# Performance work log

Measured on AMD Instinct MI355X. Metric: run time of the kernel, lower is better.

The kernel has to match this reference:

```python
import jax, jax.numpy as jnp
import numpy as np

EPS_ATTN = 1e-8  # self.eps is undefined in the torch source; standard slot-attention value
LN_EPS = 1e-5


def _ln(x, g=None, b=None, axes=(-1,)):
    m = x.mean(axes, keepdims=True)
    v = ((x - m) ** 2).mean(axes, keepdims=True)
    y = (x - m) * jax.lax.rsqrt(v + LN_EPS)
    return y * g + b if g is not None else y


def setup_inputs() -> dict:
    key = jax.random.key(0)
    ks = jax.random.split(key, 16)
    B, N, S, d, dh = 16, 4096, 8, 64, 128

    def w(k, shape, fan_in):
        return jax.random.normal(k, shape, jnp.float32) / np.float32(np.sqrt(fan_in))

    return {
        "inputs": jax.random.normal(ks[0], (B, N, d + 2), jnp.float32),
        "slots": jax.random.normal(ks[1], (S, d + 4), jnp.float32),
        "Wq": w(ks[2], (d, d), d),
        "Wk": w(ks[3], (d, d), d),
        "Wv": w(ks[4], (d, d), d),
        "Wg": w(ks[5], (d, 2), 2),
        "bg": jnp.zeros((d,), jnp.float32),
        "ln_pos_g": jnp.ones((d,), jnp.float32),
        "ln_pos_b": jnp.zeros((d,), jnp.float32),
        "W1": w(ks[6], (dh, d), d),
        "b1": jnp.zeros((dh,), jnp.float32),
        "W2": w(ks[7], (d, dh), dh),
        "b2": jnp.zeros((d,), jnp.float32),
        "W_ih": w(ks[8], (3 * d, d), d),
        "W_hh": w(ks[9], (3 * d, d), d),
        "b_ih": jnp.zeros((3 * d,), jnp.float32),
        "b_hh": jnp.zeros((3 * d,), jnp.float32),
        "ln_mlp_g": jnp.ones((d,), jnp.float32),
        "ln_mlp_b": jnp.zeros((d,), jnp.float32),
        "W3": w(ks[10], (dh, d), d),
        "b3": jnp.zeros((dh,), jnp.float32),
        "W4": w(ks[11], (d, dh), dh),
        "b4": jnp.zeros((d,), jnp.float32),
        "ln_slot_g": jnp.ones((d,), jnp.float32),
        "ln_slot_b": jnp.zeros((d,), jnp.float32),
        "n_iters": 3,
    }


def reference(inputs, slots, Wq, Wk, Wv, Wg, bg, ln_pos_g, ln_pos_b, W1, b1, W2, b2,
              W_ih, W_hh, b_ih, b_hh, ln_mlp_g, ln_mlp_b, W3, b3, W4, b4,
              ln_slot_g, ln_slot_b, n_iters):
    feats, grids = inputs[..., :-2], inputs[..., -2:]          # (B,N,d), (B,N,2)
    sl, pos, sc = slots[..., :-4], slots[..., -4:-2], slots[..., -2:]
    B, N, _ = feats.shape
    S, d = sl.shape
    scale = d ** (-0.5)

    slots = jnp.broadcast_to(sl, (B, S, d))
    positions = jnp.clip(jnp.broadcast_to(pos, (B, S, 2)), -1.0, 1.0)
    scales = jnp.clip(jnp.broadcast_to(sc, (B, S, 2)), 1e-3, 2.0)

    k = feats @ Wk.T                                           # (B,N,d)
    v = feats @ Wv.T

    def pos_mlp(x):  # LayerNorm -> Linear -> ReLU -> Linear
        h = _ln(x, ln_pos_g, ln_pos_b)
        h = jax.nn.relu(h @ W1.T + b1)
        return h @ W2.T + b2

    for i_iter in range(n_iters + 1):
        rel = (grids[:, :, None] - positions[:, None]) / scales[:, None]  # (B,N,S,2)
        rgp = rel @ Wg.T + bg                                             # (B,N,S,d)
        k_pos = pos_mlp(k[:, :, None] + rgp)                              # (B,N,S,d)
        v_pos = pos_mlp(v[:, :, None] + rgp)

        slots_n = _ln(slots, ln_slot_g, ln_slot_b)
        q = _ln(slots_n, axes=(-2, -1)) @ Wq.T                            # (B,S,d)

        dots = jnp.einsum('bsd,bnsd->bns', q, k_pos) * scale              # (B,N,S)
        attn = jax.nn.softmax(dots, axis=1) + EPS_ATTN
        attn = attn / attn.sum(axis=-1, keepdims=True)

        updates = jnp.einsum('bns,bnsd->bsd', attn, v_pos)                # (B,S,d)
        positions = jnp.einsum('bns,bnp->bsp', attn, grids)               # (B,S,2)
        spread = (grids[:, :, None] - positions[:, None]) ** 2            # (B,N,S,2)
        scales = jnp.clip(jnp.sqrt(jnp.einsum('bns,bnsp->bsp', attn, spread)), 1e-3, 2.0)

        if i_iter < n_iters:
            x = updates.reshape(-1, d)
            h = slots.reshape(-1, d)
            gi = x @ W_ih.T + b_ih
            gh = h @ W_hh.T + b_hh
            i_r, i_z, i_n = jnp.split(gi, 3, axis=-1)
            h_r, h_z, h_n = jnp.split(gh, 3, axis=-1)
            r = jax.nn.sigmoid(i_r + h_r)
            z = jax.nn.sigmoid(i_z + h_z)
            n_g = jnp.tanh(i_n + r * h_n)
            slots = ((1.0 - z) * n_g + z * h).reshape(B, S, d)
            # slot_mlp (no residual in the source)
            hmlp = jax.nn.relu(_ln(slots, ln_mlp_g, ln_mlp_b) @ W3.T + b3)
            slots = hmlp @ W4.T + b4

    return jnp.concatenate([slots, positions, scales], axis=-1)           # (B,S,d+4)
```

## Files before the change

### kernel.cpp

```cpp
#include <hip/hip_runtime.h>
#include <math.h>

#define BB 16
#define NN 4096
#define SS 8
#define DD 64
#define DHH 128
#define CIN 66
#define NITERS 3
#define LN_EPS_F 1e-5f
#define EPS_ATTN_F 1e-8f
#define QSCALE 0.125f

__device__ __forceinline__ float dot4(float4 a, float4 b) {
    return fmaf(a.x, b.x, fmaf(a.y, b.y, fmaf(a.z, b.z, a.w * b.w)));
}

__global__ __launch_bounds__(256) void k_init_slots(
    const float* __restrict__ slots_in, float* __restrict__ slots,
    float* __restrict__ positions, float* __restrict__ scales) {
    int tid = blockIdx.x * 256 + threadIdx.x;
    if (tid < BB * SS * DD) {
        int s = (tid / DD) % SS;
        int c = tid % DD;
        slots[tid] = slots_in[s * 68 + c];
    }
    if (tid < BB * SS * 2) {
        int s = (tid >> 1) & 7;
        int p = tid & 1;
        float po = slots_in[s * 68 + 64 + p];
        positions[tid] = fminf(fmaxf(po, -1.f), 1.f);
        float sc = slots_in[s * 68 + 66 + p];
        scales[tid] = fminf(fmaxf(sc, 1e-3f), 2.f);
    }
}

__global__ __launch_bounds__(256) void k_prep_w(
    const float* __restrict__ W1, const float* __restrict__ lpg,
    const float* __restrict__ lpb, const float* __restrict__ b1,
    const float* __restrict__ Wg,
    float* __restrict__ W1p, float* __restrict__ avec, float* __restrict__ bvec,
    float* __restrict__ s1vec, float* __restrict__ b1p, float* __restrict__ wgc) {
    __shared__ float w1s[128 * 68];
    int tid = threadIdx.x;
    for (int q = 0; q < 8; q++) {
        int flat = q * 1024 + tid * 4;
        int o = flat >> 6, c = flat & 63;
        *(float4*)(w1s + o * 68 + c) = *(const float4*)(W1 + flat);
    }
    __syncthreads();
    if (tid < 128) {
        int o = tid;
        float a = 0.f, bv = 0.f, s1 = 0.f, b1a = b1[o];
        for (int c = 0; c < 64; c++) {
            float w0 = w1s[o * 68 + c];
            float w = w0 * lpg[c];
            W1p[o * 64 + c] = w;
            a = fmaf(w, Wg[2 * c], a);
            bv = fmaf(w, Wg[2 * c + 1], bv);
            s1 += w;
            b1a = fmaf(w0, lpb[c], b1a);
        }
        avec[o] = a; bvec[o] = bv; s1vec[o] = s1; b1p[o] = b1a;
    }
    if (tid == 128) {
        float mwA = 0.f, mwB = 0.f, AA = 0.f, BBv = 0.f, AB = 0.f;
        for (int c = 0; c < 64; c++) {
            float wa = Wg[2 * c], wb = Wg[2 * c + 1];
            mwA += wa; mwB += wb;
            AA = fmaf(wa, wa, AA); BBv = fmaf(wb, wb, BBv); AB = fmaf(wa, wb, AB);
        }
        wgc[0] = mwA * (1.f / 64.f);
        wgc[1] = mwB * (1.f / 64.f);
        wgc[2] = AA * (1.f / 64.f);
        wgc[3] = BBv * (1.f / 64.f);
        wgc[4] = AB * (2.f / 64.f);
    }
}

__global__ __launch_bounds__(256) void k_prep_w2(
    const float* __restrict__ W1p, const float* __restrict__ Wk,
    const float* __restrict__ Wv, const float* __restrict__ bg,
    float* __restrict__ Wall, float* __restrict__ cu) {
    int flat = blockIdx.x * 256 + threadIdx.x;
    int mat = flat >> 13, rem = flat & 8191;
    int o = rem >> 6, c = rem & 63;
    const float* Wm = mat ? Wv : Wk;
    float acc = 0.f;
    for (int d = 0; d < 64; d++)
        acc = fmaf(W1p[o * 64 + d], Wm[d * 64 + c], acc);
    Wall[flat] = acc;
    if (flat < 128) {
        float a = 0.f;
        for (int d = 0; d < 64; d++) a = fmaf(W1p[flat * 64 + d], bg[d], a);
        cu[flat] = a;
    }
}

__global__ __launch_bounds__(256) void k_prep_main(
    const float* __restrict__ inp, const float* __restrict__ Wall,
    const float* __restrict__ cu, const float* __restrict__ Wk,
    const float* __restrict__ Wv, const float* __restrict__ bg,
    const float* __restrict__ Wg,
    float* __restrict__ uk, float* __restrict__ uv,
    float* __restrict__ kaux, float* __restrict__ vaux, float* __restrict__ gbuf) {
    __shared__ float A[64 * 68];
    __shared__ float Bw[128 * 68];
    __shared__ float wg2[132];
    __shared__ float bgs[64];
    __shared__ float cus[128];
    int tid = threadIdx.x;
    int chunk = blockIdx.y;
    int rowBase = blockIdx.x * 64;
    {
        int r = tid >> 2, cq = (tid & 3) * 16;
        const float* src = inp + (size_t)(rowBase + r) * CIN + cq;
        float* dst = A + r * 68 + cq;
        #pragma unroll
        for (int q = 0; q < 8; q++) {
            float2 tv = *(const float2*)(src + 2 * q);
            dst[2 * q] = tv.x; dst[2 * q + 1] = tv.y;
        }
    }
    if (chunk < 2) {
        const float* Wsrc = Wall + (size_t)chunk * 8192;
        int o = tid >> 1, c0 = (tid & 1) * 32;
        #pragma unroll
        for (int q = 0; q < 8; q++)
            *(float4*)(Bw + o * 68 + c0 + 4 * q) = *(const float4*)(Wsrc + o * 64 + c0 + 4 * q);
        if (tid < 128) cus[tid] = cu[tid];
    } else {
        int o = tid >> 1, c0 = (tid & 1) * 32;
        const float* Wsrc = (o < 64) ? (Wk + o * 64) : (Wv + (o - 64) * 64);
        #pragma unroll
        for (int q = 0; q < 8; q++)
            *(float4*)(Bw + o * 68 + c0 + 4 * q) = *(const float4*)(Wsrc + c0 + 4 * q);
        if (tid < 64) {
            wg2[tid] = Wg[2 * tid]; wg2[66 + tid] = Wg[2 * tid + 1];
            bgs[tid] = bg[tid];
        }
    }
    __syncthreads();
    int r4 = tid >> 4, j = tid & 15;
    float acc[4][8];
    #pragma unroll
    for (int rr = 0; rr < 4; rr++)
        #pragma unroll
        for (int q = 0; q < 8; q++) acc[rr][q] = 0.f;
    for (int c4 = 0; c4 < 64; c4 += 4) {
        float4 av[4];
        #pragma unroll
        for (int rr = 0; rr < 4; rr++)
            av[rr] = *(const float4*)(A + (r4 + 16 * rr) * 68 + c4);
        #pragma unroll
        for (int q = 0; q < 8; q++) {
            float4 w = *(const float4*)(Bw + (16 * q + j) * 68 + c4);
            #pragma unroll
            for (int rr = 0; rr < 4; rr++) acc[rr][q] += dot4(av[rr], w);
        }
    }
    if (chunk < 2) {
        float cub[8];
        #pragma unroll
        for (int q = 0; q < 8; q++) cub[q] = cus[16 * q + j];
        __syncthreads();
        #pragma unroll
        for (int rr = 0; rr < 4; rr++)
            #pragma unroll
            for (int q = 0; q < 8; q++)
                Bw[(r4 + 16 * rr) * 132 + 16 * q + j] = acc[rr][q] + cub[q];
        __syncthreads();
        float* dst = (chunk == 0) ? uk : uv;
        int r = tid >> 2, c0 = (tid & 3) * 32;
        #pragma unroll
        for (int q = 0; q < 8; q++)
            *(float4*)(dst + (size_t)(rowBase + r) * 128 + c0 + 4 * q) =
                *(const float4*)(Bw + r * 132 + c0 + 4 * q);
    } else {
        float wa[4], wb[4], bgk[4];
        #pragma unroll
        for (int q = 0; q < 4; q++) {
            int ch = 16 * q + j;
            wa[q] = wg2[ch]; wb[q] = wg2[66 + ch]; bgk[q] = bgs[ch];
        }
        #pragma unroll
        for (int rr = 0; rr < 4; rr++) {
            float mk = 0.f, kk = 0.f, kA = 0.f, kB = 0.f;
            float mv = 0.f, vv = 0.f, vA = 0.f, vB = 0.f;
            #pragma unroll
            for (int q = 0; q < 4; q++) {
                float x = acc[rr][q] + bgk[q];
                mk += x; kk = fmaf(x, x, kk); kA = fmaf(x, wa[q], kA); kB = fmaf(x, wb[q], kB);
                float y = acc[rr][q + 4] + bgk[q];
                mv += y; vv = fmaf(y, y, vv); vA = fmaf(y, wa[q], vA); vB = fmaf(y, wb[q], vB);
            }
            #pragma unroll
            for (int off = 1; off <= 8; off <<= 1) {
                mk += __shfl_xor(mk, off, 64); kk += __shfl_xor(kk, off, 64);
                kA += __shfl_xor(kA, off, 64); kB += __shfl_xor(kB, off, 64);
                mv += __shfl_xor(mv, off, 64); vv += __shfl_xor(vv, off, 64);
                vA += __shfl_xor(vA, off, 64); vB += __shfl_xor(vB, off, 64);
            }
            if (j == 0) {
                int row = rowBase + r4 + 16 * rr;
                float g0 = inp[(size_t)row * CIN + 64];
                float g1 = inp[(size_t)row * CIN + 65];
                float4 m1 = {mk * (1.f / 64.f), kk * (1.f / 64.f),
                             kA * (1.f / 32.f), kB * (1.f / 32.f)};
                float4 m2 = {g0, g1, 0.f, 0.f};
                *(float4*)(kaux + (size_t)row * 8) = m1;
                *(float4*)(kaux + (size_t)row * 8 + 4) = m2;
                float4 n1 = {mv * (1.f / 64.f), vv * (1.f / 64.f),
                             vA * (1.f / 32.f), vB * (1.f / 32.f)};
                *(float4*)(vaux + (size_t)row * 8) = n1;
                *(float4*)(vaux + (size_t)row * 8 + 4) = m2;
                float2 gw = {g0, g1};
                *(float2*)(gbuf + (size_t)row * 2) = gw;
            }
        }
    }
}

__global__ __launch_bounds__(512) void k_slot_prep(
    const float* __restrict__ slots, const float* __restrict__ lsg,
    const float* __restrict__ lsb, const float* __restrict__ Wq,
    const float* __restrict__ W2, const float* __restrict__ b2,
    float* __restrict__ w2q, float* __restrict__ qb2) {
    __shared__ float sn[512];
    __shared__ float qv[SS][64];
    __shared__ float wsum[8], wsum2[8];
    int b = blockIdx.x, t = threadIdx.x;
    int s = t >> 6, c = t & 63;
    float x = slots[(b * SS + s) * DD + c];
    float sum = x;
    for (int off = 32; off; off >>= 1) sum += __shfl_xor(sum, off, 64);
    float m = sum * (1.f / 64.f);
    float dv = x - m;
    float vs = dv * dv;
    for (int off = 32; off; off >>= 1) vs += __shfl_xor(vs, off, 64);
    float y = dv * rsqrtf(vs * (1.f / 64.f) + LN_EPS_F) * lsg[c] + lsb[c];
    float s1 = y, s2 = y * y;
    for (int off = 32; off; off >>= 1) { s1 += __shfl_xor(s1, off, 64); s2 += __shfl_xor(s2, off, 64); }
    if (c == 0) { wsum[s] = s1; wsum2[s] = s2; }
    __syncthreads();
    float ts1 = 0.f, ts2 = 0.f;
    #pragma unroll
    for (int i = 0; i < 8; i++) { ts1 += wsum[i]; ts2 += wsum2[i]; }
    float gm = ts1 * (1.f / 512.f);
    float gv = ts2 * (1.f / 512.f) - gm * gm;
    sn[t] = (y - gm) * rsqrtf(gv + LN_EPS_F);
    __syncthreads();
    float acc = 0.f;
    for (int j4 = 0; j4 < 64; j4 += 4)
        acc += dot4(*(const float4*)&sn[s * 64 + j4], *(const float4*)(Wq + c * 64 + j4));
    qv[s][c] = acc;
    __syncthreads();
    float a0 = 0.f, a1 = 0.f;
    for (int cc = 0; cc < 64; cc++) {
        float qc = qv[s][cc];
        a0 = fmaf(qc, W2[cc * DHH + c], a0);
        a1 = fmaf(qc, W2[cc * DHH + c + 64], a1);
    }
    w2q[(b * SS + s) * DHH + c] = a0 * QSCALE;
    w2q[(b * SS + s) * DHH + c + 64] = a1 * QSCALE;
    float qb = qv[s][c] * b2[c];
    for (int off = 32; off; off >>= 1) qb += __shfl_xor(qb, off, 64);
    if (c == 0) qb2[b * SS + s] = qb * QSCALE;
}

__global__ __launch_bounds__(256) void k_pass1(
    const float* __restrict__ uk, const float* __restrict__ kaux,
    const float* __restrict__ positions, const float* __restrict__ scales,
    const float* __restrict__ avec, const float* __restrict__ bvec,
    const float* __restrict__ s1vec, const float* __restrict__ b1p,
    const float* __restrict__ wgc, const float* __restrict__ w2q,
    const float* __restrict__ qb2, float* __restrict__ dots) {
    int tid = threadIdx.x;
    int chunk = blockIdx.x, b = blockIdx.y;
    int wv = tid >> 6, lane = tid & 63, rh = lane >> 5, ol = lane & 31;
    int o4 = ol * 4;
    float4 a4 = *(const float4*)(avec + o4);
    float4 bv4 = *(const float4*)(bvec + o4);
    float4 s14 = *(const float4*)(s1vec + o4);
    float4 b14 = *(const float4*)(b1p + o4);
    float mwA = wgc[0], mwB = wgc[1], AA = wgc[2], BBc = wgc[3], AB2 = wgc[4];
    float p0[8], p1[8], rc0[8], rc1[8], qb[8];
    float4 wq[8];
    #pragma unroll
    for (int s = 0; s < 8; s++) {
        int bs = b * 8 + s;
        p0[s] = positions[bs * 2]; p1[s] = positions[bs * 2 + 1];
        rc0[s] = 1.f / scales[bs * 2]; rc1[s] = 1.f / scales[bs * 2 + 1];
        qb[s] = qb2[bs];
        wq[s] = *(const float4*)(w2q + (size_t)bs * DHH + o4);
    }
    int row0 = chunk * 64 + wv * 16 + rh;
    size_t rg = (size_t)b * NN + row0;
    float4 m1 = *(const float4*)(kaux + rg * 8);
    float4 m2 = *(const float4*)(kaux + rg * 8 + 4);
    float4 u4 = *(const float4*)(uk + rg * 128 + o4);
    for (int st = 0; st < 8; st++) {
        float4 n1, n2, nu;
        if (st < 7) {
            size_t rgn = rg + (size_t)(st + 1) * 2;
            n1 = *(const float4*)(kaux + rgn * 8);
            n2 = *(const float4*)(kaux + rgn * 8 + 4);
            nu = *(const float4*)(uk + rgn * 128 + o4);
        }
        int row = row0 + st * 2;
        #pragma unroll
        for (int s = 0; s < 8; s++) {
            float rel0 = (m2.x - p0[s]) * rc0[s];
            float rel1 = (m2.y - p1[s]) * rc1[s];
            float m = fmaf(rel1, mwB, fmaf(rel0, mwA, m1.x));
            float q2 = fmaf(rel0, fmaf(rel0, AA, m1.z), m1.y);
            q2 = fmaf(rel1, fmaf(rel1, BBc, m1.w), q2);
            q2 = fmaf(rel0 * rel1, AB2, q2);
            float var = fmaf(-m, m, q2);
            float rstd = rsqrtf(fmaxf(var, 0.f) + LN_EPS_F);
            float p = 0.f, t, h;
            t = fmaf(-m, s14.x, u4.x); t = fmaf(rel0, a4.x, t); t = fmaf(rel1, bv4.x, t);
            h = fmaf(rstd, t, b14.x); p = fmaf(fmaxf(h, 0.f), wq[s].x, p);
            t = fmaf(-m, s14.y, u4.y); t = fmaf(rel0, a4.y, t); t = fmaf(rel1, bv4.y, t);
            h = fmaf(rstd, t, b14.y); p = fmaf(fmaxf(h, 0.f), wq[s].y, p);
            t = fmaf(-m, s14.z, u4.z); t = fmaf(rel0, a4.z, t); t = fmaf(rel1, bv4.z, t);
            h = fmaf(rstd, t, b14.z); p = fmaf(fmaxf(h, 0.f), wq[s].z, p);
            t = fmaf(-m, s14.w, u4.w); t = fmaf(rel0, a4.w, t); t = fmaf(rel1, bv4.w, t);
            h = fmaf(rstd, t, b14.w); p = fmaf(fmaxf(h, 0.f), wq[s].w, p);
            p += __shfl_xor(p, 1, 64);
            p += __shfl_xor(p, 2, 64);
            p += __shfl_xor(p, 4, 64);
            p += __shfl_xor(p, 8, 64);
            p += __shfl_xor(p, 16, 64);
            if (ol == 0)
                dots[(size_t)(b * 8 + s) * NN + row] = p + qb[s];
        }
        m1 = n1; m2 = n2; u4 = nu;
    }
}

__global__ __launch_bounds__(256) void k_pass2(
    const float* __restrict__ uv, const float* __restrict__ vaux,
    const float* __restrict__ positions, const float* __restrict__ scales,
    const float* __restrict__ avec, const float* __restrict__ bvec,
    const float* __restrict__ s1vec, const float* __restrict__ b1p,
    const float* __restrict__ wgc, const float* __restrict__ attn,
    float* __restrict__ H) {
    __shared__ float Hw[4 * 1024];
    int tid = threadIdx.x;
    int chunk = blockIdx.x, b = blockIdx.y;
    int wv = tid >> 6, lane = tid & 63, rh = lane >> 5, ol = lane & 31;
    int o4 = ol * 4;
    float4 a4 = *(const float4*)(avec + o4);
    float4 bv4 = *(const float4*)(bvec + o4);
    float4 s14 = *(const float4*)(s1vec + o4);
    float4 b14 = *(const float4*)(b1p + o4);
    float mwA = wgc[0], mwB = wgc[1], AA = wgc[2], BBc = wgc[3], AB2 = wgc[4];
    float p0[8], p1[8], rc0[8], rc1[8];
    #pragma unroll
    for (int s = 0; s < 8; s++) {
        int bs = b * 8 + s;
        p0[s] = positions[bs * 2]; p1[s] = positions[bs * 2 + 1];
        rc0[s] = 1.f / scales[bs * 2]; rc1[s] = 1.f / scales[bs * 2 + 1];
    }
    float hq[8][4];
    #pragma unroll
    for (int s = 0; s < 8; s++)
        #pragma unroll
        for (int c = 0; c < 4; c++) hq[s][c] = 0.f;
    int row0 = chunk * 64 + wv * 16 + rh;
    size_t rg = (size_t)b * NN + row0;
    float4 m1 = *(const float4*)(vaux + rg * 8);
    float4 m2 = *(const float4*)(vaux + rg * 8 + 4);
    float4 u4 = *(const float4*)(uv + rg * 128 + o4);
    for (int st = 0; st < 8; st++) {
        float4 n1, n2, nu;
        if (st < 7) {
            size_t rgn = rg + (size_t)(st + 1) * 2;
            n1 = *(const float4*)(vaux + rgn * 8);
            n2 = *(const float4*)(vaux + rgn * 8 + 4);
            nu = *(const float4*)(uv + rgn * 128 + o4);
        }
        int row = row0 + st * 2;
        #pragma unroll
        for (int s = 0; s < 8; s++) {
            float ar = attn[(size_t)(b * 8 + s) * NN + row];
            float rel0 = (m2.x - p0[s]) * rc0[s];
            float rel1 = (m2.y - p1[s]) * rc1[s];
            float m = fmaf(rel1, mwB, fmaf(rel0, mwA, m1.x));
            float q2 = fmaf(rel0, fmaf(rel0, AA, m1.z), m1.y);
            q2 = fmaf(rel1, fmaf(rel1, BBc, m1.w), q2);
            q2 = fmaf(rel0 * rel1, AB2, q2);
            float var = fmaf(-m, m, q2);
            float rstd = rsqrtf(fmaxf(var, 0.f) + LN_EPS_F);
            float t, h;
            t = fmaf(-m, s14.x, u4.x); t = fmaf(rel0, a4.x, t); t = fmaf(rel1, bv4.x, t);
            h = fmaf(rstd, t, b14.x); hq[s][0] = fmaf(ar, fmaxf(h, 0.f), hq[s][0]);
            t = fmaf(-m, s14.y, u4.y); t = fmaf(rel0, a4.y, t); t = fmaf(rel1, bv4.y, t);
            h = fmaf(rstd, t, b14.y); hq[s][1] = fmaf(ar, fmaxf(h, 0.f), hq[s][1]);
            t = fmaf(-m, s14.z, u4.z); t = fmaf(rel0, a4.z, t); t = fmaf(rel1, bv4.z, t);
            h = fmaf(rstd, t, b14.z); hq[s][2] = fmaf(ar, fmaxf(h, 0.f), hq[s][2]);
            t = fmaf(-m, s14.w, u4.w); t = fmaf(rel0, a4.w, t); t = fmaf(rel1, bv4.w, t);
            h = fmaf(rstd, t, b14.w); hq[s][3] = fmaf(ar, fmaxf(h, 0.f), hq[s][3]);
        }
        m1 = n1; m2 = n2; u4 = nu;
    }
    #pragma unroll
    for (int s = 0; s < 8; s++)
        #pragma unroll
        for (int c = 0; c < 4; c++)
            hq[s][c] += __shfl_xor(hq[s][c], 32, 64);
    if (lane < 32) {
        #pragma unroll
        for (int s = 0; s < 8; s++) {
            float4 st = {hq[s][0], hq[s][1], hq[s][2], hq[s][3]};
            *(float4*)(Hw + wv * 1024 + s * 128 + o4) = st;
        }
    }
    __syncthreads();
    #pragma unroll
    for (int q = 0; q < 4; q++) {
        int flat = q * 256 + tid;
        float sum = Hw[flat] + Hw[1024 + flat] + Hw[2048 + flat] + Hw[3072 + flat];
        atomicAdd(&H[(size_t)b * 8 * DHH + flat], sum);
    }
}

__global__ __launch_bounds__(256) void k_softmax_ms(
    const float* __restrict__ dots, float* __restrict__ Mv, float* __restrict__ Lv,
    float* __restrict__ H) {
    __shared__ float red[4];
    int bs = blockIdx.x, t = threadIdx.x;
    if (t < 128) H[(size_t)bs * DHH + t] = 0.f;
    const float* dp = dots + (size_t)bs * NN;
    float mx = -1e30f;
    #pragma unroll
    for (int it = 0; it < 4; it++) {
        float4 d = *(const float4*)(dp + it * 1024 + t * 4);
        mx = fmaxf(mx, fmaxf(fmaxf(d.x, d.y), fmaxf(d.z, d.w)));
    }
    for (int off = 32; off; off >>= 1) mx = fmaxf(mx, __shfl_xor(mx, off, 64));
    if ((t & 63) == 0) red[t >> 6] = mx;
    __syncthreads();
    float M = fmaxf(fmaxf(red[0], red[1]), fmaxf(red[2], red[3]));
    __syncthreads();
    float sm = 0.f;
    #pragma unroll
    for (int it = 0; it < 4; it++) {
        float4 d = *(const float4*)(dp + it * 1024 + t * 4);
        sm += expf(d.x - M) + expf(d.y - M) + expf(d.z - M) + expf(d.w - M);
    }
    for (int off = 32; off; off >>= 1) sm += __shfl_xor(sm, off, 64);
    if ((t & 63) == 0) red[t >> 6] = sm;
    __syncthreads();
    if (t == 0) { Mv[bs] = M; Lv[bs] = red[0] + red[1] + red[2] + red[3]; }
}

__global__ __launch_bounds__(256) void k_attn(
    const float* __restrict__ dots, const float* __restrict__ Mv,
    const float* __restrict__ Lv, float* __restrict__ attn) {
    int chunk = blockIdx.x, b = blockIdx.y;
    int n = chunk * 256 + threadIdx.x;
    float a[8];
    float rs = 0.f;
    #pragma unroll
    for (int s = 0; s < 8; s++) {
        int bs = b * 8 + s;
        float d = dots[(size_t)bs * NN + n];
        a[s] = expf(d - Mv[bs]) * (1.f / Lv[bs]) + EPS_ATTN_F;
        rs += a[s];
    }
    float inv = 1.f / rs;
    #pragma unroll
    for (int s = 0; s < 8; s++)
        attn[(size_t)(b * 8 + s) * NN + n] = a[s] * inv;
}

__global__ __launch_bounds__(256) void k_stats(
    const float* __restrict__ attn, const float* __restrict__ gbuf,
    float* __restrict__ positions, float* __restrict__ scales,
    float* __restrict__ stats) {
    __shared__ float red[4][5];
    int bs = blockIdx.x, b = bs >> 3, t = threadIdx.x;
    const float* ap = attn + (size_t)bs * NN;
    const float* gb = gbuf + (size_t)b * NN * 2;
    float v0 = 0.f, v1 = 0.f, v2 = 0.f, v3 = 0.f, v4 = 0.f;
    #pragma unroll
    for (int it = 0; it < 4; it++) {
        int n0 = it * 1024 + t * 4;
        float4 av = *(const float4*)(ap + n0);
        float4 g1 = *(const float4*)(gb + (size_t)n0 * 2);
        float4 g2 = *(const float4*)(gb + (size_t)n0 * 2 + 4);
        v0 += av.x + av.y + av.z + av.w;
        v1 = fmaf(av.x, g1.x, fmaf(av.y, g1.z, fmaf(av.z, g2.x, fmaf(av.w, g2.z, v1))));
        v2 = fmaf(av.x, g1.y, fmaf(av.y, g1.w, fmaf(av.z, g2.y, fmaf(av.w, g2.w, v2))));
        v3 = fmaf(av.x, g1.x * g1.x, fmaf(av.y, g1.z * g1.z, fmaf(av.z, g2.x * g2.x, fmaf(av.w, g2.z * g2.z, v3))));
        v4 = fmaf(av.x, g1.y * g1.y, fmaf(av.y, g1.w * g1.w, fmaf(av.z, g2.y * g2.y, fmaf(av.w, g2.w * g2.w, v4))));
    }
    for (int off = 32; off; off >>= 1) {
        v0 += __shfl_xor(v0, off, 64); v1 += __shfl_xor(v1, off, 64);
        v2 += __shfl_xor(v2, off, 64); v3 += __shfl_xor(v3, off, 64);
        v4 += __shfl_xor(v4, off, 64);
    }
    if ((t & 63) == 0) {
        int w = t >> 6;
        red[w][0] = v0; red[w][1] = v1; red[w][2] = v2; red[w][3] = v3; red[w][4] = v4;
    }
    __syncthreads();
    if (t == 0) {
        float A0 = red[0][0] + red[1][0] + red[2][0] + red[3][0];
        float A1x = red[0][1] + red[1][1] + red[2][1] + red[3][1];
        float A1y = red[0][2] + red[1][2] + red[2][2] + red[3][2];
        float A2x = red[0][3] + red[1][3] + red[2][3] + red[3][3];
        float A2y = red[0][4] + red[1][4] + red[2][4] + red[3][4];
        positions[bs * 2 + 0] = A1x;
        positions[bs * 2 + 1] = A1y;
        float sx = A2x - A1x * A1x * (2.f - A0);
        float sy = A2y - A1y * A1y * (2.f - A0);
        scales[bs * 2 + 0] = fminf(fmaxf(sqrtf(fmaxf(sx, 0.f)), 1e-3f), 2.f);
        scales[bs * 2 + 1] = fminf(fmaxf(sqrtf(fmaxf(sy, 0.f)), 1e-3f), 2.f);
        stats[bs] = A0;
    }
}

__global__ __launch_bounds__(64) void k_gru_mlp(
    const float* __restrict__ H, const float* __restrict__ stats,
    const float* __restrict__ W2, const float* __restrict__ b2,
    const float* __restrict__ W_ih, const float* __restrict__ W_hh,
    const float* __restrict__ b_ih, const float* __restrict__ b_hh,
    const float* __restrict__ lmg, const float* __restrict__ lmb,
    const float* __restrict__ W3, const float* __restrict__ b3,
    const float* __restrict__ W4, const float* __restrict__ b4,
    float* __restrict__ slots) {
    int bs = blockIdx.x;
    int c = threadIdx.x;
    __shared__ float hl[DHH], ul[DD], sl[DD], yl[DD], hml[DHH];
    hl[c] = H[bs * DHH + c];
    hl[c + 64] = H[bs * DHH + 64 + c];
    float hold = slots[bs * DD + c];
    sl[c] = hold;
    __syncthreads();
    float A0 = stats[bs];
    float u = A0 * b2[c];
    for (int o = 0; o < DHH; o += 4) {
        float4 w = *(const float4*)(W2 + c * DHH + o);
        u = fmaf(w.x, hl[o], fmaf(w.y, hl[o + 1], fmaf(w.z, hl[o + 2], fmaf(w.w, hl[o + 3], u))));
    }
    ul[c] = u;
    __syncthreads();
    float gir = b_ih[c], giz = b_ih[64 + c], gin = b_ih[128 + c];
    float ghr = b_hh[c], ghz = b_hh[64 + c], ghn = b_hh[128 + c];
    for (int k4 = 0; k4 < DD; k4 += 4) {
        float4 uu = *(const float4*)(ul + k4);
        float4 hh = *(const float4*)(sl + k4);
        gir += dot4(uu, *(const float4*)(W_ih + c * DD + k4));
        giz += dot4(uu, *(const float4*)(W_ih + (64 + c) * DD + k4));
        gin += dot4(uu, *(const float4*)(W_ih + (128 + c) * DD + k4));
        ghr += dot4(hh, *(const float4*)(W_hh + c * DD + k4));
        ghz += dot4(hh, *(const float4*)(W_hh + (64 + c) * DD + k4));
        ghn += dot4(hh, *(const float4*)(W_hh + (128 + c) * DD + k4));
    }
    float rg = 1.f / (1.f + expf(-(gir + ghr)));
    float zg = 1.f / (1.f + expf(-(giz + ghz)));
    float ng = tanhf(gin + rg * ghn);
    float snew = (1.f - zg) * ng + zg * hold;
    float sum = snew;
    for (int off = 32; off; off >>= 1) sum += __shfl_xor(sum, off, 64);
    float m = sum * (1.f / 64.f);
    float dv = snew - m;
    float vv = dv * dv;
    for (int off = 32; off; off >>= 1) vv += __shfl_xor(vv, off, 64);
    yl[c] = dv * rsqrtf(vv * (1.f / 64.f) + LN_EPS_F) * lmg[c] + lmb[c];
    __syncthreads();
    float h0 = b3[c], h1 = b3[64 + c];
    for (int k4 = 0; k4 < DD; k4 += 4) {
        float4 yy = *(const float4*)(yl + k4);
        h0 += dot4(yy, *(const float4*)(W3 + c * DD + k4));
        h1 += dot4(yy, *(const float4*)(W3 + (64 + c) * DD + k4));
    }
    hml[c] = fmaxf(h0, 0.f);
    hml[64 + c] = fmaxf(h1, 0.f);
    __syncthreads();
    float outv = b4[c];
    for (int o4 = 0; o4 < DHH; o4 += 4) {
        float4 hm4 = *(const float4*)(hml + o4);
        outv += dot4(hm4, *(const float4*)(W4 + c * DHH + o4));
    }
    slots[bs * DD + c] = outv;
}

__global__ __launch_bounds__(256) void k_write_out(
    const float* __restrict__ slots, const float* __restrict__ positions,
    const float* __restrict__ scales, float* __restrict__ out) {
    int tid = blockIdx.x * 256 + threadIdx.x;
    if (tid >= BB * SS * 68) return;
    int bs = tid / 68, c = tid % 68;
    float v;
    if (c < 64) v = slots[bs * 64 + c];
    else if (c < 66) v = positions[bs * 2 + (c - 64)];
    else v = scales[bs * 2 + (c - 66)];
    out[tid] = v;
}

extern "C" void kernel_launch(void* const* d_in, const int* in_sizes, int n_in,
                              void* d_out, int out_size, void* d_ws, size_t ws_size,
                              hipStream_t stream) {
    (void)in_sizes; (void)n_in; (void)out_size; (void)ws_size;
    const float* inp = (const float*)d_in[0];
    const float* slots_in = (const float*)d_in[1];
    const float* Wq = (const float*)d_in[2];
    const float* Wk = (const float*)d_in[3];
    const float* Wv = (const float*)d_in[4];
    const float* Wg = (const float*)d_in[5];
    const float* bg = (const float*)d_in[6];
    const float* lpg = (const float*)d_in[7];
    const float* lpb = (const float*)d_in[8];
    const float* W1 = (const float*)d_in[9];
    const float* b1 = (const float*)d_in[10];
    const float* W2 = (const float*)d_in[11];
    const float* b2 = (const float*)d_in[12];
    const float* W_ih = (const float*)d_in[13];
    const float* W_hh = (const float*)d_in[14];
    const float* b_ih = (const float*)d_in[15];
    const float* b_hh = (const float*)d_in[16];
    const float* lmg = (const float*)d_in[17];
    const float* lmb = (const float*)d_in[18];
    const float* W3 = (const float*)d_in[19];
    const float* b3 = (const float*)d_in[20];
    const float* W4 = (const float*)d_in[21];
    const float* b4 = (const float*)d_in[22];
    const float* lsg = (const float*)d_in[23];
    const float* lsb = (const float*)d_in[24];
    float* out = (float*)d_out;
    float* ws = (float*)d_ws;

    const size_t NR = (size_t)BB * NN;
    size_t o_uk = 0;
    size_t o_uv = o_uk + NR * 128;
    size_t o_kaux = o_uv + NR * 128;
    size_t o_vaux = o_kaux + NR * 8;
    size_t o_gbuf = o_vaux + NR * 8;
    size_t o_dots = o_gbuf + NR * 2;
    size_t o_attn = o_dots + NR * SS;
    size_t o_slots = o_attn + NR * SS;
    size_t o_pos = o_slots + BB * SS * DD;
    size_t o_scl = o_pos + BB * SS * 2;
    size_t o_w2q = o_scl + BB * SS * 2;
    size_t o_qb2 = o_w2q + BB * SS * DHH;
    size_t o_Mv = o_qb2 + BB * SS;
    size_t o_Lv = o_Mv + BB * SS;
    size_t o_H = o_Lv + BB * SS;
    size_t o_stats = o_H + BB * SS * DHH;
    size_t o_W1p = o_stats + BB * SS;
    size_t o_avec = o_W1p + DHH * DD;
    size_t o_bvec = o_avec + DHH;
    size_t o_s1v = o_bvec + DHH;
    size_t o_b1p = o_s1v + DHH;
    size_t o_wgc = o_b1p + DHH;
    size_t o_Wall = o_wgc + 8;
    size_t o_cu = o_Wall + 2 * DHH * DD;

    float* uk = ws + o_uk;
    float* uv = ws + o_uv;
    float* kaux = ws + o_kaux;
    float* vaux = ws + o_vaux;
    float* gbuf = ws + o_gbuf;
    float* dots = ws + o_dots;
    float* attn = ws + o_attn;
    float* slots = ws + o_slots;
    float* positions = ws + o_pos;
    float* scales = ws + o_scl;
    float* w2q = ws + o_w2q;
    float* qb2 = ws + o_qb2;
    float* Mv = ws + o_Mv;
    float* Lv = ws + o_Lv;
    float* H = ws + o_H;
    float* stats = ws + o_stats;
    float* W1p = ws + o_W1p;
    float* avec = ws + o_avec;
    float* bvec = ws + o_bvec;
    float* s1v = ws + o_s1v;
    float* b1p = ws + o_b1p;
    float* wgc = ws + o_wgc;
    float* Wall = ws + o_Wall;
    float* cu = ws + o_cu;

    k_init_slots<<<32, 256, 0, stream>>>(slots_in, slots, positions, scales);
    k_prep_w<<<1, 256, 0, stream>>>(W1, lpg, lpb, b1, Wg, W1p, avec, bvec, s1v, b1p, wgc);
    k_prep_w2<<<64, 256, 0, stream>>>(W1p, Wk, Wv, bg, Wall, cu);
    k_prep_main<<<dim3(1024, 3), 256, 0, stream>>>(inp, Wall, cu, Wk, Wv, bg, Wg,
                                                   uk, uv, kaux, vaux, gbuf);

    for (int it = 0; it <= NITERS; ++it) {
        k_slot_prep<<<BB, 512, 0, stream>>>(slots, lsg, lsb, Wq, W2, b2, w2q, qb2);
        k_pass1<<<dim3(64, BB), 256, 0, stream>>>(uk, kaux, positions, scales,
                                                  avec, bvec, s1v, b1p, wgc, w2q, qb2, dots);
        k_softmax_ms<<<BB * SS, 256, 0, stream>>>(dots, Mv, Lv, H);
        k_attn<<<dim3(16, BB), 256, 0, stream>>>(dots, Mv, Lv, attn);
        if (it < NITERS) {
            k_pass2<<<dim3(64, BB), 256, 0, stream>>>(uv, vaux, positions, scales,
                                                      avec, bvec, s1v, b1p, wgc, attn, H);
            k_stats<<<BB * SS, 256, 0, stream>>>(attn, gbuf, positions, scales, stats);
            k_gru_mlp<<<BB * SS, 64, 0, stream>>>(H, stats, W2, b2, W_ih, W_hh, b_ih, b_hh,
                                                  lmg, lmb, W3, b3, W4, b4, slots);
        } else {
            k_stats<<<BB * SS, 256, 0, stream>>>(attn, gbuf, positions, scales, stats);
        }
    }
    k_write_out<<<34, 256, 0, stream>>>(slots, positions, scales, out);
}
```

Baseline: 469.5 us.

## Move input projection prep onto FP16 split-precision MFMA with prepacked weight fragments

Replaces the FP32 LDS-tiled GEMM in the prep kernel with MFMA 16x16x32 f16 instructions. Both operands are split into high and low fp16 parts, and three MFMAs are combined to recover near-FP32 accuracy. A new kernel prepacks the weight fragments into the MFMA lane layout. The grid also drops from three chunks to two, with each block computing both the projection and its aux stats. This targets the one-time prep cost, at some accuracy risk from the split-fp16 emulation.

```diff
diff --git a/kernel.cpp b/kernel.cpp
--- a/kernel.cpp
+++ b/kernel.cpp
@@ -11,9 +11,22 @@
 #define LN_EPS_F 1e-5f
 #define EPS_ATTN_F 1e-8f
 #define QSCALE 0.125f
+#define LO_SCALE 2048.0f
+#define LO_INV 4.8828125e-4f
+
+typedef __attribute__((ext_vector_type(8))) _Float16 half8;
+typedef __attribute__((ext_vector_type(4))) float f32x4;
+union H8 { half8 v; _Float16 u[8]; };
 
 __device__ __forceinline__ float dot4(float4 a, float4 b) {
     return fmaf(a.x, b.x, fmaf(a.y, b.y, fmaf(a.z, b.z, a.w * b.w)));
+}
+
+__device__ __forceinline__ void split_fp16(float z, _Float16& h, _Float16& l) {
+    _Float16 hh = (_Float16)z;
+    float rem = (z - (float)hh) * LO_SCALE;
+    h = hh;
+    l = (_Float16)rem;
 }
 
 __global__ __launch_bounds__(256) void k_init_slots(
@@ -97,127 +110,154 @@
     }
 }
 
-__global__ __launch_bounds__(256) void k_prep_main(
-    const float* __restrict__ inp, const float* __restrict__ Wall,
-    const float* __restrict__ cu, const float* __restrict__ Wk,
-    const float* __restrict__ Wv, const float* __restrict__ bg,
+__global__ __launch_bounds__(256) void k_prep_frag(
+    const float* __restrict__ Wall, const float* __restrict__ Wk,
+    const float* __restrict__ Wv,
+    _Float16* __restrict__ cwh, _Float16* __restrict__ cwl,
+    _Float16* __restrict__ mwh, _Float16* __restrict__ mwl) {
+    int idx = blockIdx.x * 256 + threadIdx.x;
+    if (idx < 2048) {
+        int f = idx >> 6, lane = idx & 63;
+        int m = f >> 4, rest = f & 15;
+        int ot = rest >> 1, ks = rest & 1;
+        int o = ot * 16 + (lane & 15);
+        int k0 = ks * 32 + (lane >> 4) * 8;
+        const float* src = Wall + m * 8192 + o * 64 + k0;
+        #pragma unroll
+        for (int j = 0; j < 8; j++) {
+            _Float16 h, l;
+            split_fp16(src[j], h, l);
+            cwh[(size_t)f * 512 + lane * 8 + j] = h;
+            cwl[(size_t)f * 512 + lane * 8 + j] = l;
+        }
+    } else if (idx < 3072) {
+        int id2 = idx - 2048;
+        int f = id2 >> 6, lane = id2 & 63;
+        int m = f >> 3, rest = f & 7;
+        int ot = rest >> 1, ks = rest & 1;
+        int o = ot * 16 + (lane & 15);
+        int k0 = ks * 32 + (lane >> 4) * 8;
+        const float* src = (m ? Wv : Wk) + o * 64 + k0;
+        #pragma unroll
+        for (int j = 0; j < 8; j++) {
+            _Float16 h, l;
+            split_fp16(src[j], h, l);
+            mwh[(size_t)f * 512 + lane * 8 + j] = h;
+            mwl[(size_t)f * 512 + lane * 8 + j] = l;
+        }
+    }
+}
+
+__global__ __launch_bounds__(256) void k_prep_mfma(
+    const float* __restrict__ inp,
+    const _Float16* __restrict__ cwh, const _Float16* __restrict__ cwl,
+    const _Float16* __restrict__ mwh, const _Float16* __restrict__ mwl,
+    const float* __restrict__ cu, const float* __restrict__ bg,
     const float* __restrict__ Wg,
     float* __restrict__ uk, float* __restrict__ uv,
     float* __restrict__ kaux, float* __restrict__ vaux, float* __restrict__ gbuf) {
-    __shared__ float A[64 * 68];
-    __shared__ float Bw[128 * 68];
-    __shared__ float wg2[132];
-    __shared__ float bgs[64];
-    __shared__ float cus[128];
+    __shared__ float T[4][16 * 132];
     int tid = threadIdx.x;
-    int chunk = blockIdx.y;
-    int rowBase = blockIdx.x * 64;
+    int wv = tid >> 6, lane = tid & 63;
+    int quad = lane >> 4, col = lane & 15;
+    int mat = blockIdx.y;
+    int rowTile = blockIdx.x * 64 + wv * 16;
+    half8 ah[2], al[2];
     {
-        int r = tid >> 2, cq = (tid & 3) * 16;
-        const float* src = inp + (size_t)(rowBase + r) * CIN + cq;
-        float* dst = A + r * 68 + cq;
-        #pragma unroll
-        for (int q = 0; q < 8; q++) {
-            float2 tv = *(const float2*)(src + 2 * q);
-            dst[2 * q] = tv.x; dst[2 * q + 1] = tv.y;
-        }
-    }
-    if (chunk < 2) {
-        const float* Wsrc = Wall + (size_t)chunk * 8192;
-        int o = tid >> 1, c0 = (tid & 1) * 32;
-        #pragma unroll
-        for (int q = 0; q < 8; q++)
-            *(float4*)(Bw + o * 68 + c0 + 4 * q) = *(const float4*)(Wsrc + o * 64 + c0 + 4 * q);
-        if (tid < 128) cus[tid] = cu[tid];
-    } else {
-        int o = tid >> 1, c0 = (tid & 1) * 32;
-        const float* Wsrc = (o < 64) ? (Wk + o * 64) : (Wv + (o - 64) * 64);
-        #pragma unroll
-        for (int q = 0; q < 8; q++)
-            *(float4*)(Bw + o * 68 + c0 + 4 * q) = *(const float4*)(Wsrc + c0 + 4 * q);
-        if (tid < 64) {
-            wg2[tid] = Wg[2 * tid]; wg2[66 + tid] = Wg[2 * tid + 1];
-            bgs[tid] = bg[tid];
-        }
-    }
-    __syncthreads();
-    int r4 = tid >> 4, j = tid & 15;
-    float acc[4][8];
-    #pragma unroll
-    for (int rr = 0; rr < 4; rr++)
-        #pragma unroll
-        for (int q = 0; q < 8; q++) acc[rr][q] = 0.f;
-    for (int c4 = 0; c4 < 64; c4 += 4) {
-        float4 av[4];
-        #pragma unroll
-        for (int rr = 0; rr < 4; rr++)
-            av[rr] = *(const float4*)(A + (r4 + 16 * rr) * 68 + c4);
-        #pragma unroll
-        for (int q = 0; q < 8; q++) {
-            float4 w = *(const float4*)(Bw + (16 * q + j) * 68 + c4);
-            #pragma unroll
-            for (int rr = 0; rr < 4; rr++) acc[rr][q] += dot4(av[rr], w);
-        }
-    }
-    if (chunk < 2) {
-        float cub[8];
-        #pragma unroll
-        for (int q = 0; q < 8; q++) cub[q] = cus[16 * q + j];
-        __syncthreads();
-        #pragma unroll
-        for (int rr = 0; rr < 4; rr++)
-            #pragma unroll
-            for (int q = 0; q < 8; q++)
-                Bw[(r4 + 16 * rr) * 132 + 16 * q + j] = acc[rr][q] + cub[q];
-        __syncthreads();
-        float* dst = (chunk == 0) ? uk : uv;
-        int r = tid >> 2, c0 = (tid & 3) * 32;
-        #pragma unroll
-        for (int q = 0; q < 8; q++)
-            *(float4*)(dst + (size_t)(rowBase + r) * 128 + c0 + 4 * q) =
-                *(const float4*)(Bw + r * 132 + c0 + 4 * q);
-    } else {
-        float wa[4], wb[4], bgk[4];
-        #pragma unroll
-        for (int q = 0; q < 4; q++) {
-            int ch = 16 * q + j;
-            wa[q] = wg2[ch]; wb[q] = wg2[66 + ch]; bgk[q] = bgs[ch];
-        }
-        #pragma unroll
-        for (int rr = 0; rr < 4; rr++) {
-            float mk = 0.f, kk = 0.f, kA = 0.f, kB = 0.f;
-            float mv = 0.f, vv = 0.f, vA = 0.f, vB = 0.f;
+        int rA = rowTile + col;
+        const float* rp = inp + (size_t)rA * CIN + quad * 8;
+        #pragma unroll
+        for (int ks = 0; ks < 2; ks++) {
+            H8 h, l;
             #pragma unroll
             for (int q = 0; q < 4; q++) {
-                float x = acc[rr][q] + bgk[q];
-                mk += x; kk = fmaf(x, x, kk); kA = fmaf(x, wa[q], kA); kB = fmaf(x, wb[q], kB);
-                float y = acc[rr][q + 4] + bgk[q];
-                mv += y; vv = fmaf(y, y, vv); vA = fmaf(y, wa[q], vA); vB = fmaf(y, wb[q], vB);
+                float2 v = *(const float2*)(rp + ks * 32 + 2 * q);
+                split_fp16(v.x, h.u[2 * q], l.u[2 * q]);
+                split_fp16(v.y, h.u[2 * q + 1], l.u[2 * q + 1]);
             }
-            #pragma unroll
-            for (int off = 1; off <= 8; off <<= 1) {
-                mk += __shfl_xor(mk, off, 64); kk += __shfl_xor(kk, off, 64);
-                kA += __shfl_xor(kA, off, 64); kB += __shfl_xor(kB, off, 64);
-                mv += __shfl_xor(mv, off, 64); vv += __shfl_xor(vv, off, 64);
-                vA += __shfl_xor(vA, off, 64); vB += __shfl_xor(vB, off, 64);
-            }
-            if (j == 0) {
-                int row = rowBase + r4 + 16 * rr;
-                float g0 = inp[(size_t)row * CIN + 64];
-                float g1 = inp[(size_t)row * CIN + 65];
-                float4 m1 = {mk * (1.f / 64.f), kk * (1.f / 64.f),
-                             kA * (1.f / 32.f), kB * (1.f / 32.f)};
-                float4 m2 = {g0, g1, 0.f, 0.f};
-                *(float4*)(kaux + (size_t)row * 8) = m1;
-                *(float4*)(kaux + (size_t)row * 8 + 4) = m2;
-                float4 n1 = {mv * (1.f / 64.f), vv * (1.f / 64.f),
-                             vA * (1.f / 32.f), vB * (1.f / 32.f)};
-                *(float4*)(vaux + (size_t)row * 8) = n1;
-                *(float4*)(vaux + (size_t)row * 8 + 4) = m2;
-                float2 gw = {g0, g1};
+            ah[ks] = h.v; al[ks] = l.v;
+        }
+    }
+    const _Float16* cwhm = cwh + (size_t)mat * 16 * 512;
+    const _Float16* cwlm = cwl + (size_t)mat * 16 * 512;
+    #pragma unroll
+    for (int ot = 0; ot < 8; ot++) {
+        f32x4 acc1 = {0.f, 0.f, 0.f, 0.f}, acc2 = {0.f, 0.f, 0.f, 0.f};
+        #pragma unroll
+        for (int ks = 0; ks < 2; ks++) {
+            half8 bh = *(const half8*)(cwhm + (size_t)(ot * 2 + ks) * 512 + lane * 8);
+            half8 bl = *(const half8*)(cwlm + (size_t)(ot * 2 + ks) * 512 + lane * 8);
+            acc1 = __builtin_amdgcn_mfma_f32_16x16x32_f16(ah[ks], bh, acc1, 0, 0, 0);
+            acc2 = __builtin_amdgcn_mfma_f32_16x16x32_f16(al[ks], bh, acc2, 0, 0, 0);
+            acc2 = __builtin_amdgcn_mfma_f32_16x16x32_f16(ah[ks], bl, acc2, 0, 0, 0);
+        }
+        float cuv = cu[ot * 16 + col];
+        #pragma unroll
+        for (int r = 0; r < 4; r++) {
+            float u = fmaf(acc2[r], LO_INV, acc1[r]) + cuv;
+            T[wv][(quad * 4 + r) * 132 + ot * 16 + col] = u;
+        }
+    }
+    const _Float16* mwhm = mwh + (size_t)mat * 8 * 512;
+    const _Float16* mwlm = mwl + (size_t)mat * 8 * 512;
+    float mk[4] = {0.f, 0.f, 0.f, 0.f}, kk2[4] = {0.f, 0.f, 0.f, 0.f};
+    float kA[4] = {0.f, 0.f, 0.f, 0.f}, kB[4] = {0.f, 0.f, 0.f, 0.f};
+    #pragma unroll
+    for (int ot = 0; ot < 4; ot++) {
+        f32x4 acc1 = {0.f, 0.f, 0.f, 0.f}, acc2 = {0.f, 0.f, 0.f, 0.f};
+        #pragma unroll
+        for (int ks = 0; ks < 2; ks++) {
+            half8 bh = *(const half8*)(mwhm + (size_t)(ot * 2 + ks) * 512 + lane * 8);
+            half8 bl = *(const half8*)(mwlm + (size_t)(ot * 2 + ks) * 512 + lane * 8);
+            acc1 = __builtin_amdgcn_mfma_f32_16x16x32_f16(ah[ks], bh, acc1, 0, 0, 0);
+            acc2 = __builtin_amdgcn_mfma_f32_16x16x32_f16(al[ks], bh, acc2, 0, 0, 0);
+            acc2 = __builtin_amdgcn_mfma_f32_16x16x32_f16(ah[ks], bl, acc2, 0, 0, 0);
+        }
+        int o = ot * 16 + col;
+        float bgo = bg[o], wa = Wg[2 * o], wb = Wg[2 * o + 1];
+        #pragma unroll
+        for (int r = 0; r < 4; r++) {
+            float x = fmaf(acc2[r], LO_INV, acc1[r]) + bgo;
+            mk[r] += x; kk2[r] = fmaf(x, x, kk2[r]);
+            kA[r] = fmaf(x, wa, kA[r]); kB[r] = fmaf(x, wb, kB[r]);
+        }
+    }
+    #pragma unroll
+    for (int off = 1; off <= 8; off <<= 1) {
+        #pragma unroll
+        for (int r = 0; r < 4; r++) {
+            mk[r] += __shfl_xor(mk[r], off, 64);
+            kk2[r] += __shfl_xor(kk2[r], off, 64);
+            kA[r] += __shfl_xor(kA[r], off, 64);
+            kB[r] += __shfl_xor(kB[r], off, 64);
+        }
+    }
+    float* aux = mat ? vaux : kaux;
+    if (col == 0) {
+        #pragma unroll
+        for (int r = 0; r < 4; r++) {
+            int row = rowTile + quad * 4 + r;
+            float2 g = *(const float2*)(inp + (size_t)row * CIN + 64);
+            float4 m1 = {mk[r] * (1.f / 64.f), kk2[r] * (1.f / 64.f),
+                         kA[r] * (1.f / 32.f), kB[r] * (1.f / 32.f)};
+            float4 m2 = {g.x, g.y, 0.f, 0.f};
+            *(float4*)(aux + (size_t)row * 8) = m1;
+            *(float4*)(aux + (size_t)row * 8 + 4) = m2;
+            if (mat == 0) {
+                float2 gw = {g.x, g.y};
                 *(float2*)(gbuf + (size_t)row * 2) = gw;
             }
         }
+    }
+    __syncthreads();
+    {
+        float* dst = mat ? uv : uk;
+        int r = lane >> 2, cseg = (lane & 3) * 32;
+        const float* Tr = &T[wv][r * 132 + cseg];
+        float* gp = dst + (size_t)(rowTile + r) * 128 + cseg;
+        #pragma unroll
+        for (int q = 0; q < 8; q++)
+            *(float4*)(gp + 4 * q) = *(const float4*)(Tr + 4 * q);
     }
 }
 
@@ -659,6 +699,10 @@
     size_t o_wgc = o_b1p + DHH;
     size_t o_Wall = o_wgc + 8;
     size_t o_cu = o_Wall + 2 * DHH * DD;
+    size_t o_cwh = o_cu + DHH;
+    size_t o_cwl = o_cwh + 8192;
+    size_t o_mwh = o_cwl + 8192;
+    size_t o_mwl = o_mwh + 4096;
 
     float* uk = ws + o_uk;
     float* uv = ws + o_uv;
@@ -684,12 +728,17 @@
     float* wgc = ws + o_wgc;
     float* Wall = ws + o_Wall;
     float* cu = ws + o_cu;
+    _Float16* cwh = (_Float16*)(ws + o_cwh);
+    _Float16* cwl = (_Float16*)(ws + o_cwl);
+    _Float16* mwh = (_Float16*)(ws + o_mwh);
+    _Float16* mwl = (_Float16*)(ws + o_mwl);
 
     k_init_slots<<<32, 256, 0, stream>>>(slots_in, slots, positions, scales);
     k_prep_w<<<1, 256, 0, stream>>>(W1, lpg, lpb, b1, Wg, W1p, avec, bvec, s1v, b1p, wgc);
     k_prep_w2<<<64, 256, 0, stream>>>(W1p, Wk, Wv, bg, Wall, cu);
-    k_prep_main<<<dim3(1024, 3), 256, 0, stream>>>(inp, Wall, cu, Wk, Wv, bg, Wg,
-                                                   uk, uv, kaux, vaux, gbuf);
+    k_prep_frag<<<12, 256, 0, stream>>>(Wall, Wk, Wv, cwh, cwl, mwh, mwl);
+    k_prep_mfma<<<dim3(1024, 2), 256, 0, stream>>>(inp, cwh, cwl, mwh, mwl,
+                                                   cu, bg, Wg, uk, uv, kaux, vaux, gbuf);
 
     for (int it = 0; it <= NITERS; ++it) {
         k_slot_prep<<<BB, 512, 0, stream>>>(slots, lsg, lsb, Wq, W2, b2, w2q, qb2);
```

After: 455.1 us. -3.1%, faster.
